# Kernel optimization log

Hardware: AMD Instinct MI355X
Metric: run time of the kernel (lower is better)

## Reference

```python
import jax, jax.numpy as jnp
import numpy as np

M, A, B, L = 3, 4, 2048, 7   # metapaths, instances-per-example, examples, path length (edges)
H = 256                       # hidden_size
V_N, V_E = 50000, 16          # node / edge vocab
EMB_RANGE = 14.0 / H          # gdel / hidden_size


def setup_inputs() -> dict:
    key = jax.random.key(0)
    ks = jax.random.split(key, 12)
    return {
        "tokens": jax.random.randint(ks[0], (M, A, B, L + 1), 0, V_N),
        "edge_tokens": jax.random.randint(ks[1], (M, A, B, L), 0, V_E),
        "node_emb": jax.random.uniform(ks[2], (V_N, H), minval=-EMB_RANGE, maxval=EMB_RANGE, dtype=jnp.float32),
        "edge_emb": jax.random.uniform(ks[3], (V_E, H // 2), minval=-EMB_RANGE, maxval=EMB_RANGE, dtype=jnp.float32),
        "scale_W": jax.random.normal(ks[4], (H, H), dtype=jnp.float32) * 0.05,
        "scale_b": jnp.zeros((H,), jnp.float32),
        "attn_W": jax.random.normal(ks[5], (2 * H, 2 * H), dtype=jnp.float32) * 0.05,
        "attn_b": jnp.zeros((2 * H,), jnp.float32),
        "intra_context": jax.random.uniform(ks[6], (2 * H,), dtype=jnp.float32),
        "inter_W": jax.random.normal(ks[7], (2 * H, 2 * H), dtype=jnp.float32) * 0.05,
        "inter_b": jnp.zeros((2 * H,), jnp.float32),
        "inter_context": jax.random.uniform(ks[8], (2 * H,), dtype=jnp.float32),
        "out_W": jax.random.normal(ks[9], (2 * H, H), dtype=jnp.float32) * 0.05,
        "out_b": jnp.zeros((H,), jnp.float32),
    }


def _forward(tokens, edge_tokens, node_emb, edge_emb, scale_W, scale_b,
             attn_W, attn_b, intra_context, inter_W, inter_b, inter_context,
             out_W, out_b):
    Mm, Aa, Bb, Lp1 = tokens.shape
    Ll = Lp1 - 1
    Hh = node_emb.shape[1]
    per_mp = []
    for m in range(Mm):                       # small fixed metapath count
        tok = tokens[m].reshape(-1, Lp1)      # [N, L+1], N = A*B
        etok = edge_tokens[m].reshape(-1, Ll) # [N, L]
        # embed_and_scale (dropout = identity at eval); one node type -> shared table/fc
        inputs = node_emb[tok] @ scale_W + scale_b   # [N, L+1, H]
        edge_in = edge_emb[etok]                     # [N, L, H/2]
        # rotational_encoding: reversed suffix scan with RotatE-style complex rotation
        hidden = inputs
        for i in reversed(range(Ll)):
            hr, hi = jnp.split(hidden[:, i + 1:, :], 2, axis=2)   # [N, L-i, H/2]
            ir, ii = jnp.split(inputs[:, i, :], 2, axis=1)        # [N, H/2]
            er = jnp.cos(edge_in[:, i])[:, None, :]
            ei = jnp.sin(edge_in[:, i])[:, None, :]
            out_r = ir[:, None, :] + er * hr - ei * hi
            out_i = ii[:, None, :] + ei * hr + er * hi
            hidden = hidden.at[:, i + 1:, :].set(jnp.concatenate([out_r, out_i], axis=2))
        path_lens = 1.0 + jnp.arange(Lp1, dtype=hidden.dtype)
        hidden = hidden / path_lens[None, :, None]
        # cat source node rep with each suffix rep -> [N, L, 2H]
        h_all = jnp.concatenate(
            [jnp.broadcast_to(hidden[:, :1, :], (hidden.shape[0], Ll, Hh)), hidden[:, 1:, :]],
            axis=2)
        # LstmAttn with use_rnn=False, full mask, static context
        act = jnp.tanh(h_all @ attn_W + attn_b)                   # [N, L, 2H]
        w = jax.nn.softmax(act @ intra_context, axis=1)           # [N, L]
        mh = jax.nn.relu(jnp.sum(h_all * w[:, :, None], axis=1))  # [N, 2H]
        per_mp.append(mh.reshape(Aa, Bb, 2 * Hh).sum(axis=0))     # [B, 2H]
    hid = jnp.stack(per_mp, axis=1)                               # [B, M, 2H]
    # inter-metapath attention: tanh(fc) averaged over batch, scored vs context
    h_act = jnp.tanh(hid @ inter_W + inter_b).mean(axis=0)        # [M, 2H]
    scores = h_act @ inter_context                                # [M]
    out = jnp.sum(hid * scores[None, :, None], axis=1)            # [B, 2H]
    return out @ out_W + out_b                                    # [B, H]


def reference(tokens, edge_tokens, node_emb, edge_emb, scale_W, scale_b,
              attn_W, attn_b, intra_context, inter_W, inter_b, inter_context,
              out_W, out_b):
    return _forward(tokens, edge_tokens, node_emb, edge_emb, scale_W, scale_b,
                    attn_W, attn_b, intra_context, inter_W, inter_b, inter_context,
                    out_W, out_b)
```

## Files before the change

kernel.cpp:

```cpp
#include <hip/hip_runtime.h>
#include <hip/hip_bf16.h>

typedef __bf16 bf16;
typedef bf16 bf16x8 __attribute__((ext_vector_type(8)));
typedef float f32x4 __attribute__((ext_vector_type(4)));

#define MFMA16(a, b, c) __builtin_amdgcn_mfma_f32_16x16x32_bf16((a), (b), (c), 0, 0, 0)

#define MM 3
#define AA 4
#define BB 2048
#define LL 7
#define HH 256
#define VN 50000

__device__ __forceinline__ float ftanh(float x) {
    float e = __expf(2.f * x);
    float r = __builtin_amdgcn_rcpf(e + 1.f);
    return 1.f - 2.f * r;
}
__device__ __forceinline__ float bf2f(unsigned u) {
    union { unsigned u; float f; } x; x.u = u << 16; return x.f;
}
__device__ __forceinline__ unsigned f2bf(float f) {
    bf16 b = (bf16)f;
    return (unsigned)__builtin_bit_cast(unsigned short, b);
}

__global__ void prep_kernel(const float* __restrict__ scale_W, const float* __restrict__ attn_W,
                            const float* __restrict__ inter_W, const float* __restrict__ out_W,
                            const float* __restrict__ edge_emb,
                            bf16* __restrict__ scale_WT, bf16* __restrict__ WtopT,
                            bf16* __restrict__ WbotT, bf16* __restrict__ inter_WT,
                            bf16* __restrict__ out_WT,
                            float* __restrict__ ce, float* __restrict__ se,
                            float* __restrict__ S) {
    int idx = blockIdx.x * blockDim.x + threadIdx.x;
    int stride = gridDim.x * blockDim.x;
    for (int i = idx; i < 256 * 256; i += stride) {
        int k = i >> 8, c = i & 255;
        scale_WT[c * 256 + k] = (bf16)scale_W[i];
    }
    for (int i = idx; i < 512 * 256; i += stride) {
        int c = i >> 8, k = i & 255;
        WtopT[c * 256 + k] = (bf16)attn_W[k * 512 + c];
        WbotT[c * 256 + k] = (bf16)attn_W[(256 + k) * 512 + c];
    }
    for (int i = idx; i < 512 * 512; i += stride) {
        int k = i >> 9, c = i & 511;
        inter_WT[c * 512 + k] = (bf16)inter_W[i];
    }
    for (int i = idx; i < 512 * 256; i += stride) {
        int k = i >> 8, c = i & 255;
        out_WT[c * 512 + k] = (bf16)out_W[i];
    }
    for (int i = idx; i < 16 * 128; i += stride) {
        float e = edge_emb[i];
        ce[i] = cosf(e);
        se[i] = sinf(e);
    }
    for (int i = idx; i < 3 * 512; i += stride) S[i] = 0.f;
}

__global__ __launch_bounds__(512, 4) void emb_gemm_kernel(
    const float* __restrict__ node_emb, const bf16* __restrict__ scale_WT,
    const float* __restrict__ scale_b, bf16* __restrict__ scaled_emb) {
    extern __shared__ char smem[];
    bf16* Al = (bf16*)smem;
    const int tid = threadIdx.x;
    const int vb = blockIdx.x * 64;
    const int w = tid >> 6, l = tid & 63, lr = l & 15, g = l >> 4;

    bf16x8 wf[8][2];
#pragma unroll
    for (int ks = 0; ks < 8; ++ks)
#pragma unroll
        for (int ct = 0; ct < 2; ++ct)
            wf[ks][ct] = *(const bf16x8*)(scale_WT + (size_t)(w * 32 + ct * 16 + lr) * 256 +
                                          ks * 32 + g * 8);
    float bia[2];
#pragma unroll
    for (int ct = 0; ct < 2; ++ct) bia[ct] = scale_b[w * 32 + ct * 16 + lr];

    for (int it = 0; it < 8; ++it) {
        int i = tid + it * 512;
        int r = i >> 6, kq = i & 63;
        int v = vb + r;
        float4 x = (v < VN) ? *(const float4*)(node_emb + (size_t)v * 256 + kq * 4)
                            : make_float4(0.f, 0.f, 0.f, 0.f);
        bf16* d = Al + r * 264 + kq * 4;
        d[0] = (bf16)x.x; d[1] = (bf16)x.y; d[2] = (bf16)x.z; d[3] = (bf16)x.w;
    }
    __syncthreads();

    for (int rt = 0; rt < 4; ++rt) {
        f32x4 acc[2] = {};
#pragma unroll
        for (int ks = 0; ks < 8; ++ks) {
            bf16x8 aF = *(const bf16x8*)(Al + (rt * 16 + lr) * 264 + ks * 32 + g * 8);
#pragma unroll
            for (int ct = 0; ct < 2; ++ct) acc[ct] = MFMA16(aF, wf[ks][ct], acc[ct]);
        }
#pragma unroll
        for (int ct = 0; ct < 2; ++ct) {
            int col = w * 32 + ct * 16 + lr;
#pragma unroll
            for (int i2 = 0; i2 < 4; ++i2) {
                int v = vb + rt * 16 + g * 4 + i2;
                if (v < VN) scaled_emb[(size_t)v * 256 + col] = (bf16)(acc[ct][i2] + bia[ct]);
            }
        }
    }
}

__global__ __launch_bounds__(256) void scan_kernel(
    const int* __restrict__ tokens, const int* __restrict__ etok,
    const bf16* __restrict__ scaled_emb, const float* __restrict__ ce,
    const float* __restrict__ se, bf16* __restrict__ scanned, int m0) {
    const int tid = threadIdx.x;
    const int n_l = blockIdx.x * 4 + (tid >> 6);
    const int cp = tid & 63, c0 = cp * 2;
    const int b = n_l & 2047, a = (n_l >> 11) & 3, mrel = n_l >> 13;
    const int base = ((m0 + mrel) * AA + a) * BB + b;
    const int* tk = tokens + (base << 3);
    const int* eb = etok + base * LL;
    bf16* orow = scanned + (size_t)n_l * 2048;

    unsigned x0r = *(const unsigned*)(scaled_emb + (size_t)tk[0] * 256 + c0);
    unsigned x0i = *(const unsigned*)(scaled_emb + (size_t)tk[0] * 256 + c0 + 128);
    *(unsigned*)(orow + c0) = x0r;
    *(unsigned*)(orow + c0 + 128) = x0i;
    float Sr0 = bf2f(x0r & 0xffffu), Sr1 = bf2f(x0r >> 16);
    float Si0 = bf2f(x0i & 0xffffu), Si1 = bf2f(x0i >> 16);
    float P0r = 1.f, P0i = 0.f, P1r = 1.f, P1i = 0.f;
#pragma unroll
    for (int k = 1; k <= LL; ++k) {
        int e = eb[k - 1];
        int v = tk[k];
        float2 crv = *(const float2*)(ce + e * 128 + c0);
        float2 civ = *(const float2*)(se + e * 128 + c0);
        float t0r = P0r * crv.x - P0i * civ.x, t0i = P0r * civ.x + P0i * crv.x;
        float t1r = P1r * crv.y - P1i * civ.y, t1i = P1r * civ.y + P1i * crv.y;
        P0r = t0r; P0i = t0i; P1r = t1r; P1i = t1i;
        unsigned xr = *(const unsigned*)(scaled_emb + (size_t)v * 256 + c0);
        unsigned xi = *(const unsigned*)(scaled_emb + (size_t)v * 256 + c0 + 128);
        float xr0 = bf2f(xr & 0xffffu), xr1 = bf2f(xr >> 16);
        float xi0 = bf2f(xi & 0xffffu), xi1 = bf2f(xi >> 16);
        Sr0 += P0r * xr0 - P0i * xi0; Si0 += P0r * xi0 + P0i * xr0;
        Sr1 += P1r * xr1 - P1i * xi1; Si1 += P1r * xi1 + P1i * xr1;
        float inv = 1.f / (float)(k + 1);
        *(unsigned*)(orow + k * 256 + c0) = f2bf(Sr0 * inv) | (f2bf(Sr1 * inv) << 16);
        *(unsigned*)(orow + k * 256 + c0 + 128) = f2bf(Si0 * inv) | (f2bf(Si1 * inv) << 16);
    }
}

__global__ __launch_bounds__(512, 4) void attn_kernel(
    const bf16* __restrict__ scanned, const bf16* __restrict__ WtopT,
    const bf16* __restrict__ WbotT, const float* __restrict__ attn_b,
    const float* __restrict__ ctx, float* __restrict__ wsm, int m0) {
    extern __shared__ char smem[];
    bf16* Als = (bf16*)smem;
    bf16* h0l = (bf16*)(smem + 65536);
    float* lg2 = (float*)(smem + 73984);
    const int tid = threadIdx.x;
    const int w = tid >> 6, l = tid & 63, lr = l & 15, g = l >> 4;
    const int n_l0 = blockIdx.x * 16;
    const bf16* src = scanned + (size_t)n_l0 * 2048;

    for (int it = 0; it < 8; ++it) {
        int i = tid + it * 512;
        int row = i >> 5, Lch = i & 31;
        bf16x8 x = *(const bf16x8*)(src + (size_t)i * 8);
        int pch = (Lch & 24) | ((Lch & 7) ^ (row & 7));
        *(bf16x8*)(Als + row * 256 + pch * 8) = x;
        if ((row & 7) == 0) *(bf16x8*)(h0l + (row >> 3) * 264 + Lch * 8) = x;
    }
    __syncthreads();

    const int bsel = g >> 1;
    float pv[8][4] = {};
#pragma unroll 1
    for (int cc = 0; cc < 4; ++cc) {
        const int cb = cc * 128 + w * 16;
        f32x4 a0 = {};
        {
            bf16x8 wt[8];
#pragma unroll
            for (int ks = 0; ks < 8; ++ks)
                wt[ks] = *(const bf16x8*)(WtopT + (size_t)(cb + lr) * 256 + ks * 32 + g * 8);
#pragma unroll
            for (int ks = 0; ks < 8; ++ks) {
                bf16x8 aF = *(const bf16x8*)(h0l + lr * 264 + ks * 32 + g * 8);
                a0 = MFMA16(aF, wt[ks], a0);
            }
        }
        float y0sel[8];
#pragma unroll
        for (int rt = 0; rt < 8; ++rt) {
            float t0 = __shfl(a0[(2 * rt) & 3], (((2 * rt) >> 2) << 4) + lr, 64);
            float t1 = __shfl(a0[(2 * rt + 1) & 3], (((2 * rt + 1) >> 2) << 4) + lr, 64);
            y0sel[rt] = bsel ? t1 : t0;
        }
        bf16x8 wb[8];
#pragma unroll
        for (int ks = 0; ks < 8; ++ks)
            wb[ks] = *(const bf16x8*)(WbotT + (size_t)(cb + lr) * 256 + ks * 32 + g * 8);
        float bia = attn_b[cb + lr];
        float cxv = ctx[cb + lr];
#pragma unroll
        for (int rt = 0; rt < 8; ++rt) {
            float y0v = y0sel[rt];
            f32x4 accE, accO;
            accE[0] = y0v; accE[1] = y0v; accE[2] = y0v; accE[3] = y0v;
            accO[0] = 0.f; accO[1] = 0.f; accO[2] = 0.f; accO[3] = 0.f;
            __builtin_amdgcn_s_setprio(1);
#pragma unroll
            for (int ks = 0; ks < 4; ++ks) {
                bf16x8 aE = *(const bf16x8*)(Als + (rt * 16 + lr) * 256 +
                                             ((((2 * ks) * 4 + g) ^ (lr & 7)) << 3));
                bf16x8 aO = *(const bf16x8*)(Als + (rt * 16 + lr) * 256 +
                                             ((((2 * ks + 1) * 4 + g) ^ (lr & 7)) << 3));
                accE = MFMA16(aE, wb[2 * ks], accE);
                accO = MFMA16(aO, wb[2 * ks + 1], accO);
            }
            __builtin_amdgcn_s_setprio(0);
#pragma unroll
            for (int i2 = 0; i2 < 4; ++i2)
                pv[rt][i2] += cxv * ftanh(accE[i2] + accO[i2] + bia);
        }
        __builtin_amdgcn_sched_barrier(0);
    }
#pragma unroll
    for (int msk = 1; msk < 16; msk <<= 1)
#pragma unroll
        for (int rt = 0; rt < 8; ++rt)
#pragma unroll
            for (int i2 = 0; i2 < 4; ++i2) pv[rt][i2] += __shfl_xor(pv[rt][i2], msk, 64);
    if (lr == 0) {
#pragma unroll
        for (int rt = 0; rt < 8; ++rt)
#pragma unroll
            for (int i2 = 0; i2 < 4; ++i2) {
                int row = rt * 16 + g * 4 + i2;
                if (row & 7) lg2[row * 9 + w] = pv[rt][i2];
            }
    }
    __syncthreads();

    if (tid < 16) {
        int np = tid;
        float lv[LL], mx = -1e30f;
#pragma unroll
        for (int j = 1; j <= LL; ++j) {
            float sv = 0.f;
#pragma unroll
            for (int w8 = 0; w8 < 8; ++w8) sv += lg2[(np * 8 + j) * 9 + w8];
            lv[j - 1] = sv;
            mx = fmaxf(mx, sv);
        }
        float ssum = 0.f, ev[LL];
#pragma unroll
        for (int j = 0; j < LL; ++j) { ev[j] = __expf(lv[j] - mx); ssum += ev[j]; }
        float inv = 1.f / ssum;
        size_t n_g = (size_t)m0 * 8192 + n_l0 + np;
#pragma unroll
        for (int j = 0; j < LL; ++j) wsm[n_g * 8 + j + 1] = ev[j] * inv;
    }
}

__global__ __launch_bounds__(256) void wsum_kernel(
    const bf16* __restrict__ scanned, const float* __restrict__ wsm,
    float* __restrict__ hid, int m0) {
    const int b = blockIdx.x, mrel = blockIdx.y;
    const int m = m0 + mrel;
    const int tid = threadIdx.x;
    const int c0 = tid * 2;
    float acc0 = 0.f, acc1 = 0.f;
    if (c0 < 256) {
#pragma unroll
        for (int a = 0; a < AA; ++a) {
            int n_l = (mrel * AA + a) * BB + b;
            unsigned u = *(const unsigned*)(scanned + (size_t)n_l * 2048 + c0);
            acc0 += fmaxf(0.f, bf2f(u & 0xffffu));
            acc1 += fmaxf(0.f, bf2f(u >> 16));
        }
    } else {
        int cb2 = c0 - 256;
#pragma unroll
        for (int a = 0; a < AA; ++a) {
            int n_l = (mrel * AA + a) * BB + b;
            size_t n_g = (size_t)(m * AA + a) * BB + b;
            float s0 = 0.f, s1 = 0.f;
#pragma unroll
            for (int j = 1; j <= LL; ++j) {
                unsigned u = *(const unsigned*)(scanned + (size_t)n_l * 2048 + j * 256 + cb2);
                float wj = wsm[n_g * 8 + j];
                s0 += wj * bf2f(u & 0xffffu);
                s1 += wj * bf2f(u >> 16);
            }
            acc0 += fmaxf(0.f, s0);
            acc1 += fmaxf(0.f, s1);
        }
    }
    float2 o; o.x = acc0; o.y = acc1;
    *(float2*)(hid + ((size_t)b * 3 + m) * 512 + c0) = o;
}

__global__ __launch_bounds__(1024, 4) void inter_kernel(
    const float* __restrict__ hid, const bf16* __restrict__ inter_WT,
    const float* __restrict__ inter_b, float* __restrict__ S) {
    extern __shared__ char smem[];
    bf16* Al = (bf16*)smem;
    const int tid = threadIdx.x;
    const int m = blockIdx.y, rb = blockIdx.x * 32;
    const int w = tid >> 6, l = tid & 63, lr = l & 15, g = l >> 4;
    for (int it = 0; it < 4; ++it) {
        int i = tid + it * 1024;
        int r = i >> 7, kq = i & 127;
        float4 x = *(const float4*)(hid + ((size_t)(rb + r) * 3 + m) * 512 + kq * 4);
        bf16* d = Al + r * 520 + kq * 4;
        d[0] = (bf16)x.x; d[1] = (bf16)x.y; d[2] = (bf16)x.z; d[3] = (bf16)x.w;
    }
    __syncthreads();
#pragma unroll 1
    for (int cc = 0; cc < 2; ++cc) {
        int c = cc * 256 + w * 16 + lr;
        bf16x8 wf[16];
#pragma unroll
        for (int ks = 0; ks < 16; ++ks)
            wf[ks] = *(const bf16x8*)(inter_WT + (size_t)c * 512 + ks * 32 + g * 8);
        float biav = inter_b[c];
        float csum = 0.f;
        for (int rt = 0; rt < 2; ++rt) {
            f32x4 acc = {};
#pragma unroll
            for (int ks = 0; ks < 16; ++ks) {
                bf16x8 aF = *(const bf16x8*)(Al + (rt * 16 + lr) * 520 + ks * 32 + g * 8);
                acc = MFMA16(aF, wf[ks], acc);
            }
#pragma unroll
            for (int i2 = 0; i2 < 4; ++i2) csum += ftanh(acc[i2] + biav);
        }
        csum += __shfl_xor(csum, 16, 64);
        csum += __shfl_xor(csum, 32, 64);
        if (g == 0) atomicAdd(&S[m * 512 + c], csum);
        __builtin_amdgcn_sched_barrier(0);
    }
}

__global__ void scores_kernel(const float* __restrict__ S, const float* __restrict__ ictx2,
                              float* __restrict__ scores) {
    __shared__ float red[512];
    int t = threadIdx.x;
    for (int m = 0; m < 3; ++m) {
        red[t] = S[m * 512 + t] * ictx2[t];
        __syncthreads();
        for (int st = 256; st > 0; st >>= 1) {
            if (t < st) red[t] += red[t + st];
            __syncthreads();
        }
        if (t == 0) scores[m] = red[0] * (1.f / 2048.f);
        __syncthreads();
    }
}

__global__ __launch_bounds__(1024, 4) void out_kernel(
    const float* __restrict__ hid, const float* __restrict__ scores,
    const bf16* __restrict__ out_WT, const float* __restrict__ out_b,
    float* __restrict__ out) {
    extern __shared__ char smem[];
    bf16* Al = (bf16*)smem;
    const int tid = threadIdx.x;
    const int rb = blockIdx.x * 32;
    const int w = tid >> 6, l = tid & 63, lr = l & 15, g = l >> 4;
    float s0 = scores[0], s1 = scores[1], s2 = scores[2];
    for (int it = 0; it < 4; ++it) {
        int i = tid + it * 1024;
        int r = i >> 7, kq = i & 127;
        const float* hp = hid + (size_t)(rb + r) * 1536 + kq * 4;
        float4 x0 = *(const float4*)(hp);
        float4 x1 = *(const float4*)(hp + 512);
        float4 x2 = *(const float4*)(hp + 1024);
        bf16* d = Al + r * 520 + kq * 4;
        d[0] = (bf16)(x0.x * s0 + x1.x * s1 + x2.x * s2);
        d[1] = (bf16)(x0.y * s0 + x1.y * s1 + x2.y * s2);
        d[2] = (bf16)(x0.z * s0 + x1.z * s1 + x2.z * s2);
        d[3] = (bf16)(x0.w * s0 + x1.w * s1 + x2.w * s2);
    }
    __syncthreads();
    int c = w * 16 + lr;
    bf16x8 wf[16];
#pragma unroll
    for (int ks = 0; ks < 16; ++ks)
        wf[ks] = *(const bf16x8*)(out_WT + (size_t)c * 512 + ks * 32 + g * 8);
    float biav = out_b[c];
    for (int rt = 0; rt < 2; ++rt) {
        f32x4 acc = {};
#pragma unroll
        for (int ks = 0; ks < 16; ++ks) {
            bf16x8 aF = *(const bf16x8*)(Al + (rt * 16 + lr) * 520 + ks * 32 + g * 8);
            acc = MFMA16(aF, wf[ks], acc);
        }
#pragma unroll
        for (int i2 = 0; i2 < 4; ++i2)
            out[(size_t)(rb + rt * 16 + g * 4 + i2) * 256 + c] = acc[i2] + biav;
    }
}

extern "C" void kernel_launch(void* const* d_in, const int* in_sizes, int n_in,
                              void* d_out, int out_size, void* d_ws, size_t ws_size,
                              hipStream_t stream) {
    const int* tokens = (const int*)d_in[0];
    const int* etok = (const int*)d_in[1];
    const float* node_emb = (const float*)d_in[2];
    const float* edge_emb = (const float*)d_in[3];
    const float* scale_W = (const float*)d_in[4];
    const float* scale_b = (const float*)d_in[5];
    const float* attn_W = (const float*)d_in[6];
    const float* attn_b = (const float*)d_in[7];
    const float* ictx = (const float*)d_in[8];
    const float* inter_W = (const float*)d_in[9];
    const float* inter_b = (const float*)d_in[10];
    const float* ictx2 = (const float*)d_in[11];
    const float* out_W = (const float*)d_in[12];
    const float* out_b = (const float*)d_in[13];
    float* out = (float*)d_out;
    char* ws = (char*)d_ws;

    size_t off = 0;
    bf16* scale_WT = (bf16*)(ws + off); off += 256 * 256 * 2;
    bf16* WtopT = (bf16*)(ws + off);    off += 512 * 256 * 2;
    bf16* WbotT = (bf16*)(ws + off);    off += 512 * 256 * 2;
    bf16* inter_WT = (bf16*)(ws + off); off += 512 * 512 * 2;
    bf16* out_WT = (bf16*)(ws + off);   off += 512 * 256 * 2;
    float* ce = (float*)(ws + off);     off += 16 * 128 * 4;
    float* se = (float*)(ws + off);     off += 16 * 128 * 4;
    float* S = (float*)(ws + off);      off += 3 * 512 * 4;
    float* scores = (float*)(ws + off); off += 256;
    bf16* scaled_emb = (bf16*)(ws + off); off += (size_t)VN * 256 * 2;
    float* hid = (float*)(ws + off);    off += (size_t)BB * 3 * 512 * 4;
    float* wsm = (float*)(ws + off);    off += (size_t)24576 * 8 * 4;
    bf16* scanned = (bf16*)(ws + off);
    const size_t chunk_bytes = (size_t)8192 * 8 * 256 * 2;
    size_t need3 = off + chunk_bytes;
    size_t need1 = off + 3 * chunk_bytes;
    if (ws_size < need3) return;
    const int nm = (ws_size >= need1) ? 3 : 1;

    const int lds_k1 = 64 * 264 * 2;
    const int lds_B = 78592;
    const int lds_k4 = 32 * 520 * 2;
    (void)hipFuncSetAttribute((const void*)attn_kernel,
                              hipFuncAttributeMaxDynamicSharedMemorySize, lds_B);

    prep_kernel<<<1024, 256, 0, stream>>>(scale_W, attn_W, inter_W, out_W, edge_emb,
                                          scale_WT, WtopT, WbotT, inter_WT, out_WT, ce, se, S);
    emb_gemm_kernel<<<(VN + 63) / 64, 512, lds_k1, stream>>>(node_emb, scale_WT, scale_b,
                                                             scaled_emb);
    for (int m0 = 0; m0 < 3; m0 += nm) {
        scan_kernel<<<nm * 2048, 256, 0, stream>>>(tokens, etok, scaled_emb, ce, se,
                                                   scanned, m0);
        attn_kernel<<<nm * 512, 512, lds_B, stream>>>(scanned, WtopT, WbotT, attn_b, ictx,
                                                      wsm, m0);
        wsum_kernel<<<dim3(BB, nm), 256, 0, stream>>>(scanned, wsm, hid, m0);
    }
    inter_kernel<<<dim3(BB / 32, MM), 1024, lds_k4, stream>>>(hid, inter_WT, inter_b, S);
    scores_kernel<<<1, 512, 0, stream>>>(S, ictx2, scores);
    out_kernel<<<BB / 32, 1024, lds_k4, stream>>>(hid, scores, out_WT, out_b, out);
}
```

Measured before the change: 232.0 us.

## Fuse weighted-sum pooling into attention kernel by regrouping rows per example

Each attention block now loads the 16 path rows for 4 examples across all 4 instances, rather than 16 consecutive instances. This lets it compute the softmax-weighted sum, relu and instance reduction directly from LDS and write hid. The separate wsum kernel and the wsm buffer are removed, which avoids re-reading the scanned tensor from global memory and saves a launch. The cost is strided global loads across instances and a longer attention kernel with an extra LDS phase.

```diff
diff --git a/kernel.cpp b/kernel.cpp
--- a/kernel.cpp
+++ b/kernel.cpp
@@ -157,23 +157,28 @@
 __global__ __launch_bounds__(512, 4) void attn_kernel(
     const bf16* __restrict__ scanned, const bf16* __restrict__ WtopT,
     const bf16* __restrict__ WbotT, const float* __restrict__ attn_b,
-    const float* __restrict__ ctx, float* __restrict__ wsm, int m0) {
+    const float* __restrict__ ctx, float* __restrict__ hid, int m0) {
     extern __shared__ char smem[];
     bf16* Als = (bf16*)smem;
     bf16* h0l = (bf16*)(smem + 65536);
     float* lg2 = (float*)(smem + 73984);
     const int tid = threadIdx.x;
     const int w = tid >> 6, l = tid & 63, lr = l & 15, g = l >> 4;
-    const int n_l0 = blockIdx.x * 16;
-    const bf16* src = scanned + (size_t)n_l0 * 2048;
+    const int bg = blockIdx.x;
+    const int mrel = bg >> 9;
+    const int b0 = (bg & 511) * 4;
+    const int m = m0 + mrel;
 
     for (int it = 0; it < 8; ++it) {
         int i = tid + it * 512;
         int row = i >> 5, Lch = i & 31;
-        bf16x8 x = *(const bf16x8*)(src + (size_t)i * 8);
-        int pch = (Lch & 24) | ((Lch & 7) ^ (row & 7));
+        int q = row >> 3, p = row & 7;
+        int a = q >> 2, bi = q & 3;
+        const bf16* rp = scanned + ((size_t)(mrel * AA + a) * BB + b0 + bi) * 2048 + p * 256;
+        bf16x8 x = *(const bf16x8*)(rp + Lch * 8);
+        int pch = (Lch & 24) | ((Lch & 7) ^ p);
         *(bf16x8*)(Als + row * 256 + pch * 8) = x;
-        if ((row & 7) == 0) *(bf16x8*)(h0l + (row >> 3) * 264 + Lch * 8) = x;
+        if (p == 0) *(bf16x8*)(h0l + q * 264 + Lch * 8) = x;
     }
     __syncthreads();
 
@@ -248,13 +253,13 @@
     __syncthreads();
 
     if (tid < 16) {
-        int np = tid;
+        int q = tid;
         float lv[LL], mx = -1e30f;
 #pragma unroll
         for (int j = 1; j <= LL; ++j) {
             float sv = 0.f;
 #pragma unroll
-            for (int w8 = 0; w8 < 8; ++w8) sv += lg2[(np * 8 + j) * 9 + w8];
+            for (int w8 = 0; w8 < 8; ++w8) sv += lg2[(q * 8 + j) * 9 + w8];
             lv[j - 1] = sv;
             mx = fmaxf(mx, sv);
         }
@@ -262,48 +267,46 @@
 #pragma unroll
         for (int j = 0; j < LL; ++j) { ev[j] = __expf(lv[j] - mx); ssum += ev[j]; }
         float inv = 1.f / ssum;
-        size_t n_g = (size_t)m0 * 8192 + n_l0 + np;
-#pragma unroll
-        for (int j = 0; j < LL; ++j) wsm[n_g * 8 + j + 1] = ev[j] * inv;
-    }
-}
-
-__global__ __launch_bounds__(256) void wsum_kernel(
-    const bf16* __restrict__ scanned, const float* __restrict__ wsm,
-    float* __restrict__ hid, int m0) {
-    const int b = blockIdx.x, mrel = blockIdx.y;
-    const int m = m0 + mrel;
-    const int tid = threadIdx.x;
-    const int c0 = tid * 2;
-    float acc0 = 0.f, acc1 = 0.f;
-    if (c0 < 256) {
-#pragma unroll
-        for (int a = 0; a < AA; ++a) {
-            int n_l = (mrel * AA + a) * BB + b;
-            unsigned u = *(const unsigned*)(scanned + (size_t)n_l * 2048 + c0);
-            acc0 += fmaxf(0.f, bf2f(u & 0xffffu));
-            acc1 += fmaxf(0.f, bf2f(u >> 16));
-        }
-    } else {
-        int cb2 = c0 - 256;
-#pragma unroll
-        for (int a = 0; a < AA; ++a) {
-            int n_l = (mrel * AA + a) * BB + b;
-            size_t n_g = (size_t)(m * AA + a) * BB + b;
-            float s0 = 0.f, s1 = 0.f;
-#pragma unroll
-            for (int j = 1; j <= LL; ++j) {
-                unsigned u = *(const unsigned*)(scanned + (size_t)n_l * 2048 + j * 256 + cb2);
-                float wj = wsm[n_g * 8 + j];
-                s0 += wj * bf2f(u & 0xffffu);
-                s1 += wj * bf2f(u >> 16);
-            }
-            acc0 += fmaxf(0.f, s0);
-            acc1 += fmaxf(0.f, s1);
-        }
-    }
-    float2 o; o.x = acc0; o.y = acc1;
-    *(float2*)(hid + ((size_t)b * 3 + m) * 512 + c0) = o;
+#pragma unroll
+        for (int j = 0; j < LL; ++j) lg2[(q * 8 + j + 1) * 9 + 8] = ev[j] * inv;
+    }
+    __syncthreads();
+
+    for (int it2 = 0; it2 < 2; ++it2) {
+        int item = tid + it2 * 512;
+        int bi = item >> 8, cp = item & 255;
+        int c0 = cp * 2;
+        float acc0 = 0.f, acc1 = 0.f;
+        if (c0 < 256) {
+#pragma unroll
+            for (int a = 0; a < AA; ++a) {
+                int q = a * 4 + bi;
+                unsigned u = *(const unsigned*)(Als + q * 2048 + c0);
+                acc0 += fmaxf(0.f, bf2f(u & 0xffffu));
+                acc1 += fmaxf(0.f, bf2f(u >> 16));
+            }
+        } else {
+            int cb2 = c0 - 256;
+            int ch = cb2 >> 3, of = cb2 & 7;
+#pragma unroll
+            for (int a = 0; a < AA; ++a) {
+                int q = a * 4 + bi;
+                float s0 = 0.f, s1 = 0.f;
+#pragma unroll
+                for (int j = 1; j <= LL; ++j) {
+                    unsigned u = *(const unsigned*)(Als + (q * 8 + j) * 256 +
+                                                    ((ch ^ j) << 3) + of);
+                    float wj = lg2[(q * 8 + j) * 9 + 8];
+                    s0 += wj * bf2f(u & 0xffffu);
+                    s1 += wj * bf2f(u >> 16);
+                }
+                acc0 += fmaxf(0.f, s0);
+                acc1 += fmaxf(0.f, s1);
+            }
+        }
+        float2 o; o.x = acc0; o.y = acc1;
+        *(float2*)(hid + ((size_t)(b0 + bi) * 3 + m) * 512 + c0) = o;
+    }
 }
 
 __global__ __launch_bounds__(1024, 4) void inter_kernel(
@@ -439,7 +442,6 @@
     float* scores = (float*)(ws + off); off += 256;
     bf16* scaled_emb = (bf16*)(ws + off); off += (size_t)VN * 256 * 2;
     float* hid = (float*)(ws + off);    off += (size_t)BB * 3 * 512 * 4;
-    float* wsm = (float*)(ws + off);    off += (size_t)24576 * 8 * 4;
     bf16* scanned = (bf16*)(ws + off);
     const size_t chunk_bytes = (size_t)8192 * 8 * 256 * 2;
     size_t need3 = off + chunk_bytes;
@@ -461,8 +463,7 @@
         scan_kernel<<<nm * 2048, 256, 0, stream>>>(tokens, etok, scaled_emb, ce, se,
                                                    scanned, m0);
         attn_kernel<<<nm * 512, 512, lds_B, stream>>>(scanned, WtopT, WbotT, attn_b, ictx,
-                                                      wsm, m0);
-        wsum_kernel<<<dim3(BB, nm), 256, 0, stream>>>(scanned, wsm, hid, m0);
+                                                      hid, m0);
     }
     inter_kernel<<<dim3(BB / 32, MM), 1024, lds_k4, stream>>>(hid, inter_WT, inter_b, S);
     scores_kernel<<<1, 512, 0, stream>>>(S, ictx2, scores);
```

After: 218.5 us, median of 2. 5.9% less time.
